# Kernel tuning notes

Hardware: AMD Instinct MI355X
Metric: run time of the kernel (lower is better)

The kernel has to match this reference:

```python
import jax, jax.numpy as jnp
import numpy as np

H = 128        # num_hidden
NIN = 384      # num_in
FF = 4 * H
SCALE = 30.0
EPS = 1e-5


def _gelu(x):
    return jax.nn.gelu(x, approximate=False)


def _layernorm(x, g, b):
    mu = jnp.mean(x, axis=-1, keepdims=True)
    var = jnp.var(x, axis=-1, keepdims=True)
    return (x - mu) * jax.lax.rsqrt(var + EPS) * g + b


def setup_inputs() -> dict:
    key = jax.random.key(0)
    ks = jax.random.split(key, 12)
    B, N, K = 4, 2048, 48
    s = lambda fan_in: 1.0 / np.sqrt(fan_in)
    inp = {
        "h_V": jax.random.normal(ks[0], (B, N, H), jnp.float32),
        "h_E": jax.random.normal(ks[1], (B, N, K, NIN), jnp.float32),
        "mask_V": jnp.ones((B, N), jnp.float32),
        "mask_attend": jnp.ones((B, N, K), jnp.float32),
        "W1_w": jax.random.uniform(ks[2], (H + NIN, H), jnp.float32, -s(H + NIN), s(H + NIN)),
        "W1_b": jnp.zeros((H,), jnp.float32),
        "W2_w": jax.random.uniform(ks[3], (H, H), jnp.float32, -s(H), s(H)),
        "W2_b": jnp.zeros((H,), jnp.float32),
        "W3_w": jax.random.uniform(ks[4], (H, H), jnp.float32, -s(H), s(H)),
        "W3_b": jnp.zeros((H,), jnp.float32),
        "Win_w": jax.random.uniform(ks[5], (H, FF), jnp.float32, -s(H), s(H)),
        "Win_b": jnp.zeros((FF,), jnp.float32),
        "Wout_w": jax.random.uniform(ks[6], (FF, H), jnp.float32, -s(FF), s(FF)),
        "Wout_b": jnp.zeros((H,), jnp.float32),
        "ln1_g": jnp.ones((H,), jnp.float32),
        "ln1_b": jnp.zeros((H,), jnp.float32),
        "ln2_g": jnp.ones((H,), jnp.float32),
        "ln2_b": jnp.zeros((H,), jnp.float32),
    }
    return inp


def reference(h_V, h_E, mask_V, mask_attend,
              W1_w, W1_b, W2_w, W2_b, W3_w, W3_b,
              Win_w, Win_b, Wout_w, Wout_b,
              ln1_g, ln1_b, ln2_g, ln2_b):
    B, N, K, _ = h_E.shape
    # expand node feats over K neighbors and concat with edge feats -> [B,N,K,H+NIN]
    h_V_expand = jnp.broadcast_to(h_V[:, :, None, :], (B, N, K, h_V.shape[-1]))
    h_EV = jnp.concatenate([h_V_expand, h_E], axis=-1)
    # edge MLP: 3 linears, 2 GELUs
    h_message = _gelu(h_EV @ W1_w + W1_b)
    h_message = _gelu(h_message @ W2_w + W2_b)
    h_message = h_message @ W3_w + W3_b
    h_message = mask_attend[..., None] * h_message
    dh = jnp.sum(h_message, axis=-2) / SCALE  # [B,N,H]
    h = _layernorm(h_V + dh, ln1_g, ln1_b)
    # position-wise FFN
    dh = _gelu(h @ Win_w + Win_b) @ Wout_w + Wout_b
    h = _layernorm(h + dh, ln2_g, ln2_b)
    h = mask_V[..., None] * h
    return h
```

## Files before the change

kernel.cpp:

```cpp
#include <hip/hip_runtime.h>
#include <hip/hip_bf16.h>

#define Hh    128
#define NINc  384
#define KN    48
#define FFd   512
#define NNODE 8192

typedef __attribute__((ext_vector_type(8))) short short8v;
typedef __attribute__((ext_vector_type(4))) float f32x4;

__device__ __forceinline__ short f2bf1(float f){
  union { __hip_bfloat16 h; short s; } c; c.h = __float2bfloat16(f);
  return c.s;
}
__device__ __forceinline__ unsigned pk_bf16(float lo, float hi){
  union { __hip_bfloat162 h; unsigned u; } c;
  c.h = __float22bfloat162_rn(make_float2(lo, hi));
  return c.u;
}

__device__ __forceinline__ float gelu_f(float x){
  float t = 0.7978845608028654f * x * (1.0f + 0.044715f * x * x);
  float e = __expf(2.0f * t);
  return x * (1.0f - 1.0f / (e + 1.0f));
}

__device__ __forceinline__ void bar_lds(){
  asm volatile("s_waitcnt lgkmcnt(0)\n\ts_barrier" ::: "memory");
}

__global__ void prep_weights(const float* __restrict__ W1, const float* __restrict__ W2,
                             const float* __restrict__ W3, const float* __restrict__ Win,
                             const float* __restrict__ Wout,
                             short* __restrict__ w1vT, short* __restrict__ w1p,
                             short* __restrict__ w2p,  short* __restrict__ w3T,
                             short* __restrict__ winT, short* __restrict__ woutT)
{
  int i = blockIdx.x * 256 + threadIdx.x;
  if (i < 16384){ int n = i / 128, k = i % 128; w1vT[i] = f2bf1(W1[k*128 + n]); return; }
  i -= 16384;
  if (i < 49152){
    int n = i / 6144, r = i % 6144;
    int ks = r / 512, r2 = r % 512;
    int lane = r2 / 8, j = r2 % 8;
    int qq = lane >> 4, arow = lane & 15;
    w1p[i] = f2bf1(W1[(128 + ks*32 + qq*8 + j)*128 + n*16 + arow]); return;
  }
  i -= 49152;
  if (i < 16384){
    int n = i / 2048, r = i % 2048;
    int ks = r / 512, r2 = r % 512;
    int lane = r2 / 8, j = r2 % 8;
    int qq = lane >> 4, arow = lane & 15;
    w2p[i] = f2bf1(W2[(ks*32 + qq*8 + j)*128 + n*16 + arow]); return;
  }
  i -= 16384;
  if (i < 16384){ int n = i / 128, k = i % 128; w3T[i] = f2bf1(W3[k*128 + n]); return; }
  i -= 16384;
  if (i < 65536){ int n = i / 128, k = i % 128; winT[i] = f2bf1(Win[k*512 + n]); return; }
  i -= 65536;
  if (i < 65536){ int n = i / 512, k = i % 512; woutT[i] = f2bf1(Wout[k*128 + n]); return; }
}

__global__ __launch_bounds__(256,4) void np_kernel(
    const float* __restrict__ hV, const short* __restrict__ w1vT,
    const float* __restrict__ b1, float* __restrict__ npart)
{
  const int row0 = blockIdx.x * 32;
  const int tid = threadIdx.x, lane = tid & 63, wv = tid >> 6;
  __shared__ __attribute__((aligned(16))) short Xs[32][Hh + 8];

  const float4* src = (const float4*)(hV + (size_t)row0 * Hh);
  #pragma unroll
  for (int j = 0; j < 4; ++j){
    int idx = tid + 256*j;
    int r = idx >> 5, c4 = idx & 31;
    float4 v = src[idx];
    *(uint2*)&Xs[r][c4*4] = make_uint2(pk_bf16(v.x,v.y), pk_bf16(v.z,v.w));
  }
  __syncthreads();

  const int arow = lane & 15, kgrp = (lane >> 4) * 8;
  const int col0 = wv * 32, ccol = lane & 15, crow0 = (lane >> 4) * 4;

  f32x4 acc[2][2];
  #pragma unroll
  for (int m = 0; m < 2; ++m) for (int n = 0; n < 2; ++n) acc[m][n] = (f32x4){0.f,0.f,0.f,0.f};

  const short8v* Bw = (const short8v*)w1vT;
  #pragma unroll
  for (int ks = 0; ks < 4; ++ks){
    int kb = ks*32 + kgrp;
    short8v b0 = Bw[(col0 + arow)*16      + (kb >> 3)];
    short8v b1f = Bw[(col0 + 16 + arow)*16 + (kb >> 3)];
    #pragma unroll
    for (int m = 0; m < 2; ++m){
      short8v a = *(const short8v*)&Xs[m*16 + arow][kb];
      acc[m][0] = __builtin_amdgcn_mfma_f32_16x16x32_bf16(a, b0,  acc[m][0], 0,0,0);
      acc[m][1] = __builtin_amdgcn_mfma_f32_16x16x32_bf16(a, b1f, acc[m][1], 0,0,0);
    }
  }
  #pragma unroll
  for (int m = 0; m < 2; ++m) for (int n = 0; n < 2; ++n){
    int colg = col0 + n*16 + ccol;
    float bb = b1[colg];
    #pragma unroll
    for (int r = 0; r < 4; ++r)
      npart[(size_t)(row0 + m*16 + crow0 + r)*Hh + colg] = acc[m][n][r] + bb;
  }
}

__global__ __launch_bounds__(256,4) void edge_kernel(
    const float* __restrict__ hE,
    const float* __restrict__ maskA, const float* __restrict__ npart,
    const short* __restrict__ w1p, const short* __restrict__ w2p,
    const float* __restrict__ b2,
    float* __restrict__ sbuf, float* __restrict__ smaskbuf)
{
  const int node = blockIdx.x;
  const int tid = threadIdx.x, lane = tid & 63, wv = tid >> 6;
  const int e = lane & 15, q = lane >> 4;
  const int n0 = wv * 32;

  __shared__ __attribute__((aligned(16))) short Et[KN][NINc + 8];
  short (*M1)[136] = (short (*)[136])&Et[0][0];

  const float4* src = (const float4*)(hE + (size_t)node * (KN*NINc));
  float4 pf[6];

  auto LOADC = [&](int c){
    #pragma unroll
    for (int j = 0; j < 6; ++j){
      int idx = tid + 256*j;
      int r = idx >> 5, c4 = idx & 31;
      pf[j] = src[r*96 + c*32 + c4];
    }
  };
  auto STOREC = [&](int c){
    #pragma unroll
    for (int j = 0; j < 6; ++j){
      int idx = tid + 256*j;
      int r = idx >> 5, c4 = idx & 31;
      *(uint2*)&Et[r][c*128 + c4*4] =
        make_uint2(pk_bf16(pf[j].x, pf[j].y), pk_bf16(pf[j].z, pf[j].w));
    }
  };

  const float4 npv0 = *(const float4*)(npart + (size_t)node*Hh + n0 + 4*q);
  const float4 npv1 = *(const float4*)(npart + (size_t)node*Hh + n0 + 16 + 4*q);
  const float4 b2v0 = *(const float4*)(b2 + n0 + 4*q);
  const float4 b2v1 = *(const float4*)(b2 + n0 + 16 + 4*q);
  const float mk0 = maskA[node*KN + e];
  const float mk1 = maskA[node*KN + 16 + e];
  const float mk2 = maskA[node*KN + 32 + e];

  const f32x4 Z = (f32x4){0.f,0.f,0.f,0.f};
  f32x4 a00=Z, a10=Z, a20=Z, a01=Z, a11=Z, a21=Z;
  const short8v* B1 = (const short8v*)w1p;

  auto G1C = [&](int c){
    #pragma unroll
    for (int kk = 0; kk < 4; ++kk){
      int ks = c*4 + kk;
      short8v f0 = B1[((2*wv  )*12 + ks)*64 + lane];
      short8v f1 = B1[((2*wv+1)*12 + ks)*64 + lane];
      int kb = ks*32 + q*8;
      short8v t0 = *(const short8v*)&Et[e][kb];
      short8v t1 = *(const short8v*)&Et[16 + e][kb];
      short8v t2 = *(const short8v*)&Et[32 + e][kb];
      a00 = __builtin_amdgcn_mfma_f32_16x16x32_bf16(f0, t0, a00, 0,0,0);
      a10 = __builtin_amdgcn_mfma_f32_16x16x32_bf16(f0, t1, a10, 0,0,0);
      a20 = __builtin_amdgcn_mfma_f32_16x16x32_bf16(f0, t2, a20, 0,0,0);
      a01 = __builtin_amdgcn_mfma_f32_16x16x32_bf16(f1, t0, a01, 0,0,0);
      a11 = __builtin_amdgcn_mfma_f32_16x16x32_bf16(f1, t1, a11, 0,0,0);
      a21 = __builtin_amdgcn_mfma_f32_16x16x32_bf16(f1, t2, a21, 0,0,0);
    }
  };

  LOADC(0);
  STOREC(0);
  LOADC(1);
  bar_lds();
  G1C(0);
  STOREC(1);
  LOADC(2);
  bar_lds();
  G1C(1);
  STOREC(2);
  bar_lds();
  G1C(2);
  bar_lds();

  #define WR_M(ACC, ET, COLB, BV)  { short4 s;                      \
    s.x = f2bf1(gelu_f(ACC[0] + BV.x));                             \
    s.y = f2bf1(gelu_f(ACC[1] + BV.y));                             \
    s.z = f2bf1(gelu_f(ACC[2] + BV.z));                             \
    s.w = f2bf1(gelu_f(ACC[3] + BV.w));                             \
    *(short4*)&M1[16*ET + e][COLB + 4*q] = s; }

  WR_M(a00, 0, n0,      npv0)  WR_M(a10, 1, n0,      npv0)
  WR_M(a20, 2, n0,      npv0)  WR_M(a01, 0, n0 + 16, npv1)
  WR_M(a11, 1, n0 + 16, npv1)  WR_M(a21, 2, n0 + 16, npv1)
  #undef WR_M
  bar_lds();

  {
    f32x4 c00=Z, c10=Z, c20=Z, c01=Z, c11=Z, c21=Z;
    const short8v* B2f = (const short8v*)w2p;
    #pragma unroll
    for (int ks = 0; ks < 4; ++ks){
      short8v f0 = B2f[((2*wv  )*4 + ks)*64 + lane];
      short8v f1 = B2f[((2*wv+1)*4 + ks)*64 + lane];
      int kb = ks*32 + q*8;
      short8v t0 = *(const short8v*)&M1[e][kb];
      short8v t1 = *(const short8v*)&M1[16 + e][kb];
      short8v t2 = *(const short8v*)&M1[32 + e][kb];
      c00 = __builtin_amdgcn_mfma_f32_16x16x32_bf16(f0, t0, c00, 0,0,0);
      c10 = __builtin_amdgcn_mfma_f32_16x16x32_bf16(f0, t1, c10, 0,0,0);
      c20 = __builtin_amdgcn_mfma_f32_16x16x32_bf16(f0, t2, c20, 0,0,0);
      c01 = __builtin_amdgcn_mfma_f32_16x16x32_bf16(f1, t0, c01, 0,0,0);
      c11 = __builtin_amdgcn_mfma_f32_16x16x32_bf16(f1, t1, c11, 0,0,0);
      c21 = __builtin_amdgcn_mfma_f32_16x16x32_bf16(f1, t2, c21, 0,0,0);
    }
    float sv0[4], sv1[4];
    #pragma unroll
    for (int r = 0; r < 4; ++r){
      sv0[r] = gelu_f(c00[r] + b2v0[r])*mk0 + gelu_f(c10[r] + b2v0[r])*mk1
             + gelu_f(c20[r] + b2v0[r])*mk2;
      sv1[r] = gelu_f(c01[r] + b2v1[r])*mk0 + gelu_f(c11[r] + b2v1[r])*mk1
             + gelu_f(c21[r] + b2v1[r])*mk2;
    }
    float m3 = mk0 + mk1 + mk2;
    #pragma unroll
    for (int s = 1; s <= 8; s <<= 1){
      #pragma unroll
      for (int r = 0; r < 4; ++r){
        sv0[r] += __shfl_xor(sv0[r], s);
        sv1[r] += __shfl_xor(sv1[r], s);
      }
      m3 += __shfl_xor(m3, s);
    }
    if (e == 0){
      float4 o0 = make_float4(sv0[0], sv0[1], sv0[2], sv0[3]);
      float4 o1 = make_float4(sv1[0], sv1[1], sv1[2], sv1[3]);
      *(float4*)(sbuf + (size_t)node*Hh + n0 + 4*q)      = o0;
      *(float4*)(sbuf + (size_t)node*Hh + n0 + 16 + 4*q) = o1;
    }
    if (tid == 0) smaskbuf[node] = m3;
  }
}

__global__ __launch_bounds__(256,4) void dh_kernel(
    const float* __restrict__ hV, const float* __restrict__ sbuf,
    const float* __restrict__ smaskbuf, const short* __restrict__ w3T,
    const float* __restrict__ b3, float* __restrict__ out)
{
  const int row0 = blockIdx.x * 32;
  const int tid = threadIdx.x, lane = tid & 63, wv = tid >> 6;
  __shared__ __attribute__((aligned(16))) short Ss[32][Hh + 8];
  __shared__ float smS[32];

  const float4* src = (const float4*)(sbuf + (size_t)row0 * Hh);
  #pragma unroll
  for (int j = 0; j < 4; ++j){
    int idx = tid + 256*j;
    int r = idx >> 5, c4 = idx & 31;
    float4 v = src[idx];
    *(uint2*)&Ss[r][c4*4] = make_uint2(pk_bf16(v.x,v.y), pk_bf16(v.z,v.w));
  }
  if (tid < 32) smS[tid] = smaskbuf[row0 + tid];
  __syncthreads();

  const int arow = lane & 15, kgrp = (lane >> 4) * 8;
  const int col0 = wv * 32, ccol = lane & 15, crow0 = (lane >> 4) * 4;

  f32x4 acc[2][2];
  #pragma unroll
  for (int m = 0; m < 2; ++m) for (int n = 0; n < 2; ++n) acc[m][n] = (f32x4){0.f,0.f,0.f,0.f};

  const short8v* Bw = (const short8v*)w3T;
  #pragma unroll
  for (int ks = 0; ks < 4; ++ks){
    int kb = ks*32 + kgrp;
    short8v b0 = Bw[(col0 + arow)*16      + (kb >> 3)];
    short8v b1f = Bw[(col0 + 16 + arow)*16 + (kb >> 3)];
    #pragma unroll
    for (int m = 0; m < 2; ++m){
      short8v a = *(const short8v*)&Ss[m*16 + arow][kb];
      acc[m][0] = __builtin_amdgcn_mfma_f32_16x16x32_bf16(a, b0,  acc[m][0], 0,0,0);
      acc[m][1] = __builtin_amdgcn_mfma_f32_16x16x32_bf16(a, b1f, acc[m][1], 0,0,0);
    }
  }
  #pragma unroll
  for (int m = 0; m < 2; ++m) for (int n = 0; n < 2; ++n){
    int colg = col0 + n*16 + ccol;
    float bb = b3[colg];
    #pragma unroll
    for (int r = 0; r < 4; ++r){
      int rl = m*16 + crow0 + r;
      size_t gi = (size_t)(row0 + rl)*Hh + colg;
      out[gi] = hV[gi] + (acc[m][n][r] + bb*smS[rl]) * (1.0f/30.0f);
    }
  }
}

__global__ __launch_bounds__(256,2) void ffn_kernel(
    const float* __restrict__ ln1g, const float* __restrict__ ln1b,
    const short* __restrict__ winT, const float* __restrict__ bin,
    const short* __restrict__ woutT, const float* __restrict__ bout,
    const float* __restrict__ ln2g, const float* __restrict__ ln2b,
    const float* __restrict__ maskV, float* __restrict__ io)
{
  const int row0 = blockIdx.x * 32;
  const int tid = threadIdx.x, lane = tid & 63, wv = tid >> 6;
  __shared__ __attribute__((aligned(16))) short Xs[32][Hh + 8];
  __shared__ __attribute__((aligned(16))) float Rs[32][Hh + 4];
  __shared__ __attribute__((aligned(16))) short Hs[32][FFd + 8];

  const int arow = lane & 15, kgrp = (lane >> 4) * 8;
  const int ccol = lane & 15, crow0 = (lane >> 4) * 4;

  {
    int r = tid >> 3, cb = (tid & 7) * 16;
    const float4* xp = (const float4*)(io + (size_t)(row0 + r)*Hh + cb);
    float xv[16];
    #pragma unroll
    for (int j = 0; j < 4; ++j){
      float4 v = xp[j];
      xv[j*4+0]=v.x; xv[j*4+1]=v.y; xv[j*4+2]=v.z; xv[j*4+3]=v.w;
    }
    float sum = 0.f, sq = 0.f;
    #pragma unroll
    for (int j = 0; j < 16; ++j){ sum += xv[j]; sq += xv[j]*xv[j]; }
    #pragma unroll
    for (int d = 1; d < 8; d <<= 1){ sum += __shfl_xor(sum, d); sq += __shfl_xor(sq, d); }
    float mu = sum * (1.0f/128.0f);
    float var = sq * (1.0f/128.0f) - mu*mu;
    float rstd = rsqrtf(var + 1e-5f);
    #pragma unroll
    for (int j = 0; j < 16; ++j){
      int c = cb + j;
      float xn = (xv[j] - mu) * rstd * ln1g[c] + ln1b[c];
      Xs[r][c] = f2bf1(xn);
      Rs[r][c] = xn;
    }
  }
  __syncthreads();

  {
    f32x4 acc[2][8];
    #pragma unroll
    for (int m = 0; m < 2; ++m) for (int n = 0; n < 8; ++n) acc[m][n] = (f32x4){0.f,0.f,0.f,0.f};
    const short8v* Bw = (const short8v*)winT;
    #pragma unroll
    for (int ks = 0; ks < 4; ++ks){
      int kb = ks*32 + kgrp;
      short8v a0 = *(const short8v*)&Xs[arow][kb];
      short8v a1 = *(const short8v*)&Xs[16 + arow][kb];
      #pragma unroll
      for (int n = 0; n < 8; ++n){
        short8v b = Bw[(wv*128 + n*16 + arow)*16 + (kb >> 3)];
        acc[0][n] = __builtin_amdgcn_mfma_f32_16x16x32_bf16(a0,b,acc[0][n],0,0,0);
        acc[1][n] = __builtin_amdgcn_mfma_f32_16x16x32_bf16(a1,b,acc[1][n],0,0,0);
      }
    }
    #pragma unroll
    for (int m = 0; m < 2; ++m) for (int n = 0; n < 8; ++n){
      int colg = wv*128 + n*16 + ccol;
      float bb = bin[colg];
      #pragma unroll
      for (int r = 0; r < 4; ++r)
        Hs[m*16 + crow0 + r][colg] = f2bf1(gelu_f(acc[m][n][r] + bb));
    }
  }
  __syncthreads();

  {
    f32x4 acc[2][2];
    #pragma unroll
    for (int m = 0; m < 2; ++m) for (int n = 0; n < 2; ++n) acc[m][n] = (f32x4){0.f,0.f,0.f,0.f};
    const short8v* Bw = (const short8v*)woutT;
    #pragma unroll
    for (int ks = 0; ks < 16; ++ks){
      int kb = ks*32 + kgrp;
      short8v a0 = *(const short8v*)&Hs[arow][kb];
      short8v a1 = *(const short8v*)&Hs[16 + arow][kb];
      short8v b0 = Bw[(wv*32 + arow)*64      + (kb >> 3)];
      short8v b1f = Bw[(wv*32 + 16 + arow)*64 + (kb >> 3)];
      acc[0][0] = __builtin_amdgcn_mfma_f32_16x16x32_bf16(a0,b0, acc[0][0],0,0,0);
      acc[1][0] = __builtin_amdgcn_mfma_f32_16x16x32_bf16(a1,b0, acc[1][0],0,0,0);
      acc[0][1] = __builtin_amdgcn_mfma_f32_16x16x32_bf16(a0,b1f,acc[0][1],0,0,0);
      acc[1][1] = __builtin_amdgcn_mfma_f32_16x16x32_bf16(a1,b1f,acc[1][1],0,0,0);
    }
    #pragma unroll
    for (int m = 0; m < 2; ++m) for (int n = 0; n < 2; ++n){
      int colg = wv*32 + n*16 + ccol;
      float bb = bout[colg];
      #pragma unroll
      for (int r = 0; r < 4; ++r){
        int rr = m*16 + crow0 + r;
        Rs[rr][colg] = Rs[rr][colg] + acc[m][n][r] + bb;
      }
    }
  }
  __syncthreads();

  {
    int r = tid >> 3, cb = (tid & 7) * 16;
    float xv[16];
    #pragma unroll
    for (int j = 0; j < 16; ++j) xv[j] = Rs[r][cb + j];
    float sum = 0.f, sq = 0.f;
    #pragma unroll
    for (int j = 0; j < 16; ++j){ sum += xv[j]; sq += xv[j]*xv[j]; }
    #pragma unroll
    for (int d = 1; d < 8; d <<= 1){ sum += __shfl_xor(sum, d); sq += __shfl_xor(sq, d); }
    float mu = sum * (1.0f/128.0f);
    float var = sq * (1.0f/128.0f) - mu*mu;
    float rstd = rsqrtf(var + 1e-5f);
    float mv = maskV[row0 + r];
    float* op = io + (size_t)(row0 + r)*Hh + cb;
    #pragma unroll
    for (int j = 0; j < 4; ++j){
      float4 o;
      o.x = ((xv[j*4+0] - mu)*rstd*ln2g[cb+j*4+0] + ln2b[cb+j*4+0]) * mv;
      o.y = ((xv[j*4+1] - mu)*rstd*ln2g[cb+j*4+1] + ln2b[cb+j*4+1]) * mv;
      o.z = ((xv[j*4+2] - mu)*rstd*ln2g[cb+j*4+2] + ln2b[cb+j*4+2]) * mv;
      o.w = ((xv[j*4+3] - mu)*rstd*ln2g[cb+j*4+3] + ln2b[cb+j*4+3]) * mv;
      ((float4*)op)[j] = o;
    }
  }
}

extern "C" void kernel_launch(void* const* d_in, const int* in_sizes, int n_in,
                              void* d_out, int out_size, void* d_ws, size_t ws_size,
                              hipStream_t stream)
{
  const float* hV    = (const float*)d_in[0];
  const float* hE    = (const float*)d_in[1];
  const float* maskV = (const float*)d_in[2];
  const float* maskA = (const float*)d_in[3];
  const float* W1w   = (const float*)d_in[4];
  const float* W1b   = (const float*)d_in[5];
  const float* W2w   = (const float*)d_in[6];
  const float* W2b   = (const float*)d_in[7];
  const float* W3w   = (const float*)d_in[8];
  const float* W3b   = (const float*)d_in[9];
  const float* Winw  = (const float*)d_in[10];
  const float* Winb  = (const float*)d_in[11];
  const float* Woutw = (const float*)d_in[12];
  const float* Woutb = (const float*)d_in[13];
  const float* l1g   = (const float*)d_in[14];
  const float* l1b   = (const float*)d_in[15];
  const float* l2g   = (const float*)d_in[16];
  const float* l2b   = (const float*)d_in[17];

  char* ws = (char*)d_ws;
  size_t off = 0;
  float* npart = (float*)(ws + off); off += (size_t)NNODE * Hh * 4;
  float* sbuf  = (float*)(ws + off); off += (size_t)NNODE * Hh * 4;
  float* smbuf = (float*)(ws + off); off += (size_t)NNODE * 4;
  short* w1vT  = (short*)(ws + off); off += 16384*2;
  short* w1p   = (short*)(ws + off); off += 49152*2;
  short* w2p   = (short*)(ws + off); off += 16384*2;
  short* w3T   = (short*)(ws + off); off += 16384*2;
  short* winT  = (short*)(ws + off); off += 65536*2;
  short* woutT = (short*)(ws + off); off += 65536*2;
  if (ws_size < off) return;

  prep_weights<<<896, 256, 0, stream>>>(W1w, W2w, W3w, Winw, Woutw,
                                        w1vT, w1p, w2p, w3T, winT, woutT);
  np_kernel<<<NNODE/32, 256, 0, stream>>>(hV, w1vT, W1b, npart);
  edge_kernel<<<NNODE, 256, 0, stream>>>(hE, maskA, npart,
                                         w1p, w2p, W2b, sbuf, smbuf);
  dh_kernel<<<NNODE/32, 256, 0, stream>>>(hV, sbuf, smbuf, w3T, W3b, (float*)d_out);
  ffn_kernel<<<NNODE/32, 256, 0, stream>>>(l1g, l1b, winT, Winb, woutT, Woutb,
                                           l2g, l2b, maskV, (float*)d_out);
}
```

Baseline: 192.0 us.

## Make edge kernel persistent with cross-node prefetch and fuse dh into FFN

The edge kernel becomes persistent over a fixed grid of 768 blocks. Each block loops over nodes and prefetches the next node's edge features into registers while it computes the current node's GEMMs. M1 now has its own LDS buffer so the staging buffer can be refilled while layer 2 runs. The dh kernel (W3 projection plus residual) is merged into the FFN kernel, which removes one launch and a global round trip of the intermediate. The cost is more LDS per block, a lower occupancy hint (launch bounds 3 instead of 4), and a fixed grid that may leave CUs unevenly loaded.

```diff
diff --git a/kernel.cpp b/kernel.cpp
--- a/kernel.cpp
+++ b/kernel.cpp
@@ -6,6 +6,7 @@
 #define KN    48
 #define FFd   512
 #define NNODE 8192
+#define EGRID 768
 
 typedef __attribute__((ext_vector_type(8))) short short8v;
 typedef __attribute__((ext_vector_type(4))) float f32x4;
@@ -111,25 +112,32 @@
   }
 }
 
-__global__ __launch_bounds__(256,4) void edge_kernel(
+__global__ __launch_bounds__(256,3) void edge_kernel(
     const float* __restrict__ hE,
     const float* __restrict__ maskA, const float* __restrict__ npart,
     const short* __restrict__ w1p, const short* __restrict__ w2p,
     const float* __restrict__ b2,
     float* __restrict__ sbuf, float* __restrict__ smaskbuf)
 {
-  const int node = blockIdx.x;
   const int tid = threadIdx.x, lane = tid & 63, wv = tid >> 6;
   const int e = lane & 15, q = lane >> 4;
   const int n0 = wv * 32;
 
   __shared__ __attribute__((aligned(16))) short Et[KN][NINc + 8];
-  short (*M1)[136] = (short (*)[136])&Et[0][0];
-
-  const float4* src = (const float4*)(hE + (size_t)node * (KN*NINc));
+  __shared__ __attribute__((aligned(16))) short M1[KN][136];
+
+  const float4 b2v0 = *(const float4*)(b2 + n0 + 4*q);
+  const float4 b2v1 = *(const float4*)(b2 + n0 + 16 + 4*q);
+  const short8v* B1  = (const short8v*)w1p;
+  const short8v* B2f = (const short8v*)w2p;
+  const f32x4 Z = (f32x4){0.f,0.f,0.f,0.f};
+
   float4 pf[6];
-
-  auto LOADC = [&](int c){
+  f32x4 a00, a10, a20, a01, a11, a21;
+
+  auto LOADC = [&](int nn, int c){
+    if (nn >= NNODE) return;
+    const float4* src = (const float4*)(hE + (size_t)nn * (KN*NINc));
     #pragma unroll
     for (int j = 0; j < 6; ++j){
       int idx = tid + 256*j;
@@ -146,19 +154,6 @@
         make_uint2(pk_bf16(pf[j].x, pf[j].y), pk_bf16(pf[j].z, pf[j].w));
     }
   };
-
-  const float4 npv0 = *(const float4*)(npart + (size_t)node*Hh + n0 + 4*q);
-  const float4 npv1 = *(const float4*)(npart + (size_t)node*Hh + n0 + 16 + 4*q);
-  const float4 b2v0 = *(const float4*)(b2 + n0 + 4*q);
-  const float4 b2v1 = *(const float4*)(b2 + n0 + 16 + 4*q);
-  const float mk0 = maskA[node*KN + e];
-  const float mk1 = maskA[node*KN + 16 + e];
-  const float mk2 = maskA[node*KN + 32 + e];
-
-  const f32x4 Z = (f32x4){0.f,0.f,0.f,0.f};
-  f32x4 a00=Z, a10=Z, a20=Z, a01=Z, a11=Z, a21=Z;
-  const short8v* B1 = (const short8v*)w1p;
-
   auto G1C = [&](int c){
     #pragma unroll
     for (int kk = 0; kk < 4; ++kk){
@@ -178,158 +173,156 @@
     }
   };
 
-  LOADC(0);
+  LOADC(blockIdx.x, 0);
   STOREC(0);
-  LOADC(1);
+  LOADC(blockIdx.x, 1);
   bar_lds();
-  G1C(0);
-  STOREC(1);
-  LOADC(2);
-  bar_lds();
-  G1C(1);
-  STOREC(2);
-  bar_lds();
-  G1C(2);
-  bar_lds();
-
-  #define WR_M(ACC, ET, COLB, BV)  { short4 s;                      \
-    s.x = f2bf1(gelu_f(ACC[0] + BV.x));                             \
-    s.y = f2bf1(gelu_f(ACC[1] + BV.y));                             \
-    s.z = f2bf1(gelu_f(ACC[2] + BV.z));                             \
-    s.w = f2bf1(gelu_f(ACC[3] + BV.w));                             \
-    *(short4*)&M1[16*ET + e][COLB + 4*q] = s; }
-
-  WR_M(a00, 0, n0,      npv0)  WR_M(a10, 1, n0,      npv0)
-  WR_M(a20, 2, n0,      npv0)  WR_M(a01, 0, n0 + 16, npv1)
-  WR_M(a11, 1, n0 + 16, npv1)  WR_M(a21, 2, n0 + 16, npv1)
-  #undef WR_M
-  bar_lds();
-
-  {
-    f32x4 c00=Z, c10=Z, c20=Z, c01=Z, c11=Z, c21=Z;
-    const short8v* B2f = (const short8v*)w2p;
-    #pragma unroll
-    for (int ks = 0; ks < 4; ++ks){
-      short8v f0 = B2f[((2*wv  )*4 + ks)*64 + lane];
-      short8v f1 = B2f[((2*wv+1)*4 + ks)*64 + lane];
-      int kb = ks*32 + q*8;
-      short8v t0 = *(const short8v*)&M1[e][kb];
-      short8v t1 = *(const short8v*)&M1[16 + e][kb];
-      short8v t2 = *(const short8v*)&M1[32 + e][kb];
-      c00 = __builtin_amdgcn_mfma_f32_16x16x32_bf16(f0, t0, c00, 0,0,0);
-      c10 = __builtin_amdgcn_mfma_f32_16x16x32_bf16(f0, t1, c10, 0,0,0);
-      c20 = __builtin_amdgcn_mfma_f32_16x16x32_bf16(f0, t2, c20, 0,0,0);
-      c01 = __builtin_amdgcn_mfma_f32_16x16x32_bf16(f1, t0, c01, 0,0,0);
-      c11 = __builtin_amdgcn_mfma_f32_16x16x32_bf16(f1, t1, c11, 0,0,0);
-      c21 = __builtin_amdgcn_mfma_f32_16x16x32_bf16(f1, t2, c21, 0,0,0);
-    }
-    float sv0[4], sv1[4];
-    #pragma unroll
-    for (int r = 0; r < 4; ++r){
-      sv0[r] = gelu_f(c00[r] + b2v0[r])*mk0 + gelu_f(c10[r] + b2v0[r])*mk1
-             + gelu_f(c20[r] + b2v0[r])*mk2;
-      sv1[r] = gelu_f(c01[r] + b2v1[r])*mk0 + gelu_f(c11[r] + b2v1[r])*mk1
-             + gelu_f(c21[r] + b2v1[r])*mk2;
-    }
-    float m3 = mk0 + mk1 + mk2;
-    #pragma unroll
-    for (int s = 1; s <= 8; s <<= 1){
+
+  for (int node = blockIdx.x; node < NNODE; node += EGRID){
+    const int nxt = node + EGRID;
+
+    const float4 npv0 = *(const float4*)(npart + (size_t)node*Hh + n0 + 4*q);
+    const float4 npv1 = *(const float4*)(npart + (size_t)node*Hh + n0 + 16 + 4*q);
+    const float mk0 = maskA[node*KN + e];
+    const float mk1 = maskA[node*KN + 16 + e];
+    const float mk2 = maskA[node*KN + 32 + e];
+
+    a00 = Z; a10 = Z; a20 = Z; a01 = Z; a11 = Z; a21 = Z;
+
+    G1C(0); STOREC(1); LOADC(node, 2); bar_lds();
+    G1C(1); STOREC(2); LOADC(nxt, 0);  bar_lds();
+    G1C(2); STOREC(0); LOADC(nxt, 1);  bar_lds();
+
+    {
+      #define WR_M(ACC, ET, COLB, BV)  { short4 s;                  \
+        s.x = f2bf1(gelu_f(ACC[0] + BV.x));                         \
+        s.y = f2bf1(gelu_f(ACC[1] + BV.y));                         \
+        s.z = f2bf1(gelu_f(ACC[2] + BV.z));                         \
+        s.w = f2bf1(gelu_f(ACC[3] + BV.w));                         \
+        *(short4*)&M1[16*ET + e][COLB + 4*q] = s; }
+      WR_M(a00, 0, n0,      npv0)  WR_M(a10, 1, n0,      npv0)
+      WR_M(a20, 2, n0,      npv0)  WR_M(a01, 0, n0 + 16, npv1)
+      WR_M(a11, 1, n0 + 16, npv1)  WR_M(a21, 2, n0 + 16, npv1)
+      #undef WR_M
+    }
+    bar_lds();
+
+    {
+      f32x4 c00=Z, c10=Z, c20=Z, c01=Z, c11=Z, c21=Z;
+      #pragma unroll
+      for (int ks = 0; ks < 4; ++ks){
+        short8v f0 = B2f[((2*wv  )*4 + ks)*64 + lane];
+        short8v f1 = B2f[((2*wv+1)*4 + ks)*64 + lane];
+        int kb = ks*32 + q*8;
+        short8v t0 = *(const short8v*)&M1[e][kb];
+        short8v t1 = *(const short8v*)&M1[16 + e][kb];
+        short8v t2 = *(const short8v*)&M1[32 + e][kb];
+        c00 = __builtin_amdgcn_mfma_f32_16x16x32_bf16(f0, t0, c00, 0,0,0);
+        c10 = __builtin_amdgcn_mfma_f32_16x16x32_bf16(f0, t1, c10, 0,0,0);
+        c20 = __builtin_amdgcn_mfma_f32_16x16x32_bf16(f0, t2, c20, 0,0,0);
+        c01 = __builtin_amdgcn_mfma_f32_16x16x32_bf16(f1, t0, c01, 0,0,0);
+        c11 = __builtin_amdgcn_mfma_f32_16x16x32_bf16(f1, t1, c11, 0,0,0);
+        c21 = __builtin_amdgcn_mfma_f32_16x16x32_bf16(f1, t2, c21, 0,0,0);
+      }
+      float sv0[4], sv1[4];
       #pragma unroll
       for (int r = 0; r < 4; ++r){
-        sv0[r] += __shfl_xor(sv0[r], s);
-        sv1[r] += __shfl_xor(sv1[r], s);
-      }
-      m3 += __shfl_xor(m3, s);
-    }
-    if (e == 0){
-      float4 o0 = make_float4(sv0[0], sv0[1], sv0[2], sv0[3]);
-      float4 o1 = make_float4(sv1[0], sv1[1], sv1[2], sv1[3]);
-      *(float4*)(sbuf + (size_t)node*Hh + n0 + 4*q)      = o0;
-      *(float4*)(sbuf + (size_t)node*Hh + n0 + 16 + 4*q) = o1;
-    }
-    if (tid == 0) smaskbuf[node] = m3;
-  }
-}
-
-__global__ __launch_bounds__(256,4) void dh_kernel(
+        sv0[r] = gelu_f(c00[r] + b2v0[r])*mk0 + gelu_f(c10[r] + b2v0[r])*mk1
+               + gelu_f(c20[r] + b2v0[r])*mk2;
+        sv1[r] = gelu_f(c01[r] + b2v1[r])*mk0 + gelu_f(c11[r] + b2v1[r])*mk1
+               + gelu_f(c21[r] + b2v1[r])*mk2;
+      }
+      float m3 = mk0 + mk1 + mk2;
+      #pragma unroll
+      for (int s = 1; s <= 8; s <<= 1){
+        #pragma unroll
+        for (int r = 0; r < 4; ++r){
+          sv0[r] += __shfl_xor(sv0[r], s);
+          sv1[r] += __shfl_xor(sv1[r], s);
+        }
+        m3 += __shfl_xor(m3, s);
+      }
+      if (e == 0){
+        *(float4*)(sbuf + (size_t)node*Hh + n0 + 4*q) =
+            make_float4(sv0[0], sv0[1], sv0[2], sv0[3]);
+        *(float4*)(sbuf + (size_t)node*Hh + n0 + 16 + 4*q) =
+            make_float4(sv1[0], sv1[1], sv1[2], sv1[3]);
+      }
+      if (tid == 0) smaskbuf[node] = m3;
+    }
+  }
+}
+
+__global__ __launch_bounds__(256,2) void ffn2_kernel(
     const float* __restrict__ hV, const float* __restrict__ sbuf,
     const float* __restrict__ smaskbuf, const short* __restrict__ w3T,
-    const float* __restrict__ b3, float* __restrict__ out)
-{
-  const int row0 = blockIdx.x * 32;
-  const int tid = threadIdx.x, lane = tid & 63, wv = tid >> 6;
-  __shared__ __attribute__((aligned(16))) short Ss[32][Hh + 8];
-  __shared__ float smS[32];
-
-  const float4* src = (const float4*)(sbuf + (size_t)row0 * Hh);
-  #pragma unroll
-  for (int j = 0; j < 4; ++j){
-    int idx = tid + 256*j;
-    int r = idx >> 5, c4 = idx & 31;
-    float4 v = src[idx];
-    *(uint2*)&Ss[r][c4*4] = make_uint2(pk_bf16(v.x,v.y), pk_bf16(v.z,v.w));
-  }
-  if (tid < 32) smS[tid] = smaskbuf[row0 + tid];
-  __syncthreads();
-
-  const int arow = lane & 15, kgrp = (lane >> 4) * 8;
-  const int col0 = wv * 32, ccol = lane & 15, crow0 = (lane >> 4) * 4;
-
-  f32x4 acc[2][2];
-  #pragma unroll
-  for (int m = 0; m < 2; ++m) for (int n = 0; n < 2; ++n) acc[m][n] = (f32x4){0.f,0.f,0.f,0.f};
-
-  const short8v* Bw = (const short8v*)w3T;
-  #pragma unroll
-  for (int ks = 0; ks < 4; ++ks){
-    int kb = ks*32 + kgrp;
-    short8v b0 = Bw[(col0 + arow)*16      + (kb >> 3)];
-    short8v b1f = Bw[(col0 + 16 + arow)*16 + (kb >> 3)];
-    #pragma unroll
-    for (int m = 0; m < 2; ++m){
-      short8v a = *(const short8v*)&Ss[m*16 + arow][kb];
-      acc[m][0] = __builtin_amdgcn_mfma_f32_16x16x32_bf16(a, b0,  acc[m][0], 0,0,0);
-      acc[m][1] = __builtin_amdgcn_mfma_f32_16x16x32_bf16(a, b1f, acc[m][1], 0,0,0);
-    }
-  }
-  #pragma unroll
-  for (int m = 0; m < 2; ++m) for (int n = 0; n < 2; ++n){
-    int colg = col0 + n*16 + ccol;
-    float bb = b3[colg];
-    #pragma unroll
-    for (int r = 0; r < 4; ++r){
-      int rl = m*16 + crow0 + r;
-      size_t gi = (size_t)(row0 + rl)*Hh + colg;
-      out[gi] = hV[gi] + (acc[m][n][r] + bb*smS[rl]) * (1.0f/30.0f);
-    }
-  }
-}
-
-__global__ __launch_bounds__(256,2) void ffn_kernel(
+    const float* __restrict__ b3,
     const float* __restrict__ ln1g, const float* __restrict__ ln1b,
     const short* __restrict__ winT, const float* __restrict__ bin,
     const short* __restrict__ woutT, const float* __restrict__ bout,
     const float* __restrict__ ln2g, const float* __restrict__ ln2b,
-    const float* __restrict__ maskV, float* __restrict__ io)
+    const float* __restrict__ maskV, float* __restrict__ out)
 {
   const int row0 = blockIdx.x * 32;
   const int tid = threadIdx.x, lane = tid & 63, wv = tid >> 6;
   __shared__ __attribute__((aligned(16))) short Xs[32][Hh + 8];
   __shared__ __attribute__((aligned(16))) float Rs[32][Hh + 4];
   __shared__ __attribute__((aligned(16))) short Hs[32][FFd + 8];
+  __shared__ float smS[32];
 
   const int arow = lane & 15, kgrp = (lane >> 4) * 8;
   const int ccol = lane & 15, crow0 = (lane >> 4) * 4;
 
   {
+    const float4* src = (const float4*)(sbuf + (size_t)row0 * Hh);
+    #pragma unroll
+    for (int j = 0; j < 4; ++j){
+      int idx = tid + 256*j;
+      int r = idx >> 5, c4 = idx & 31;
+      float4 v = src[idx];
+      *(uint2*)&Xs[r][c4*4] = make_uint2(pk_bf16(v.x,v.y), pk_bf16(v.z,v.w));
+    }
+    if (tid < 32) smS[tid] = smaskbuf[row0 + tid];
+  }
+  __syncthreads();
+
+  {
+    f32x4 acc[2][2];
+    #pragma unroll
+    for (int m = 0; m < 2; ++m) for (int n = 0; n < 2; ++n) acc[m][n] = (f32x4){0.f,0.f,0.f,0.f};
+    const short8v* Bw = (const short8v*)w3T;
+    const int col0 = wv * 32;
+    #pragma unroll
+    for (int ks = 0; ks < 4; ++ks){
+      int kb = ks*32 + kgrp;
+      short8v b0 = Bw[(col0 + arow)*16      + (kb >> 3)];
+      short8v b1f = Bw[(col0 + 16 + arow)*16 + (kb >> 3)];
+      #pragma unroll
+      for (int m = 0; m < 2; ++m){
+        short8v a = *(const short8v*)&Xs[m*16 + arow][kb];
+        acc[m][0] = __builtin_amdgcn_mfma_f32_16x16x32_bf16(a, b0,  acc[m][0], 0,0,0);
+        acc[m][1] = __builtin_amdgcn_mfma_f32_16x16x32_bf16(a, b1f, acc[m][1], 0,0,0);
+      }
+    }
+    #pragma unroll
+    for (int m = 0; m < 2; ++m) for (int n = 0; n < 2; ++n){
+      int colg = col0 + n*16 + ccol;
+      float bb = b3[colg];
+      #pragma unroll
+      for (int r = 0; r < 4; ++r){
+        int rl = m*16 + crow0 + r;
+        Rs[rl][colg] = hV[(size_t)(row0 + rl)*Hh + colg]
+                     + (acc[m][n][r] + bb*smS[rl]) * (1.0f/30.0f);
+      }
+    }
+  }
+  __syncthreads();
+
+  {
     int r = tid >> 3, cb = (tid & 7) * 16;
-    const float4* xp = (const float4*)(io + (size_t)(row0 + r)*Hh + cb);
     float xv[16];
     #pragma unroll
-    for (int j = 0; j < 4; ++j){
-      float4 v = xp[j];
-      xv[j*4+0]=v.x; xv[j*4+1]=v.y; xv[j*4+2]=v.z; xv[j*4+3]=v.w;
-    }
+    for (int j = 0; j < 16; ++j) xv[j] = Rs[r][cb + j];
     float sum = 0.f, sq = 0.f;
     #pragma unroll
     for (int j = 0; j < 16; ++j){ sum += xv[j]; sq += xv[j]*xv[j]; }
@@ -420,7 +413,7 @@
     float var = sq * (1.0f/128.0f) - mu*mu;
     float rstd = rsqrtf(var + 1e-5f);
     float mv = maskV[row0 + r];
-    float* op = io + (size_t)(row0 + r)*Hh + cb;
+    float* op = out + (size_t)(row0 + r)*Hh + cb;
     #pragma unroll
     for (int j = 0; j < 4; ++j){
       float4 o;
@@ -472,9 +465,9 @@
   prep_weights<<<896, 256, 0, stream>>>(W1w, W2w, W3w, Winw, Woutw,
                                         w1vT, w1p, w2p, w3T, winT, woutT);
   np_kernel<<<NNODE/32, 256, 0, stream>>>(hV, w1vT, W1b, npart);
-  edge_kernel<<<NNODE, 256, 0, stream>>>(hE, maskA, npart,
+  edge_kernel<<<EGRID, 256, 0, stream>>>(hE, maskA, npart,
                                          w1p, w2p, W2b, sbuf, smbuf);
-  dh_kernel<<<NNODE/32, 256, 0, stream>>>(hV, sbuf, smbuf, w3T, W3b, (float*)d_out);
-  ffn_kernel<<<NNODE/32, 256, 0, stream>>>(l1g, l1b, winT, Winb, woutT, Woutb,
-                                           l2g, l2b, maskV, (float*)d_out);
-}
+  ffn2_kernel<<<NNODE/32, 256, 0, stream>>>(hV, sbuf, smbuf, w3T, W3b,
+                                            l1g, l1b, winT, Winb, woutT, Woutb,
+                                            l2g, l2b, maskV, (float*)d_out);
+}
```

After: 280.0 us. 1.46x slower.
